# Kernel optimization log

Hardware: AMD Instinct MI355X
Metric: run time of the kernel (lower is better)

Reference implementation:

```python
import jax, jax.numpy as jnp
import numpy as np

H = 16        # num_heads
E = 1024      # embed_size
OUT = 1024    # out_dim
TEMP = 1.0
EPS = 1e-20
LN_EPS = 1e-5


def setup_inputs() -> dict:
    key = jax.random.key(0)
    ks = jax.random.split(key, 16)
    B, S = 8, 4096
    s = 1.0 / np.sqrt(E)
    inp = {
        'x': jax.random.normal(ks[0], (B, S, E), dtype=jnp.float32),
        'gumbel_u': jax.random.uniform(ks[1], (B, H, S, 2), dtype=jnp.float32, minval=1e-6, maxval=1.0 - 1e-6),
        'query': jax.random.uniform(ks[2], (1, E), dtype=jnp.float32, minval=-s, maxval=s),  # xavier-ish
        'Wq': jax.random.uniform(ks[3], (E, E), jnp.float32, -s, s),
        'bq': jnp.zeros((E,), jnp.float32),
        'Wk': jax.random.uniform(ks[4], (E, E), jnp.float32, -s, s),
        'bk': jnp.zeros((E,), jnp.float32),
        'Wv': jax.random.uniform(ks[5], (E, E), jnp.float32, -s, s),
        'bv': jnp.zeros((E,), jnp.float32),
        'ln_g': jnp.ones((E,), jnp.float32),
        'ln_b': jnp.zeros((E,), jnp.float32),
        'W1': jax.random.uniform(ks[6], (4 * E, E), jnp.float32, -s, s),
        'b1': jnp.zeros((4 * E,), jnp.float32),
        'W2': jax.random.uniform(ks[7], (OUT, 4 * E), jnp.float32, -0.5 * s, 0.5 * s),
        'b2': jnp.zeros((OUT,), jnp.float32),
    }
    return inp


def reference(x, gumbel_u, query, Wq, bq, Wk, bk, Wv, bv, ln_g, ln_b, W1, b1, W2, b2):
    B, S, _ = x.shape
    dk = E // H
    # projections
    q = (query @ Wq.T + bq).reshape(H, dk)                      # [H, dk] (single query, broadcast over batch)
    k = (x @ Wk.T + bk).reshape(B, S, H, dk)                    # [B, S, H, dk]
    v = (x @ Wv.T + bv).reshape(B, S, H, dk)
    # single-query attention logits
    logits = jnp.einsum('hd,bshd->bhs', q, k) / np.sqrt(dk)     # [B, H, S]
    probs = jax.nn.softmax(logits, axis=-1)                     # [B, H, S]
    # gumbel-softmax hard mask over {keep=0-logit, drop/keep pair}
    edges = jnp.stack([jnp.zeros_like(logits), logits], axis=-1)  # [B, H, S, 2]
    g = -jnp.log(-jnp.log(gumbel_u + EPS) + EPS)
    y_soft = jax.nn.softmax((edges + g) / TEMP, axis=-1)
    idx = jnp.argmax(y_soft, axis=-1)
    y_hard = jax.nn.one_hot(idx, 2, dtype=y_soft.dtype)
    y = jax.lax.stop_gradient(y_hard - y_soft) + y_soft         # straight-through
    A = y[..., 1]                                               # [B, H, S]
    probs = A * probs
    # weighted sum of values; merge heads (seq_len of query is 1)
    hidden = jnp.einsum('bhs,bshd->bhd', probs, v).reshape(B, E)
    # layernorm
    mu = hidden.mean(axis=-1, keepdims=True)
    var = hidden.var(axis=-1, keepdims=True)
    hidden = (hidden - mu) / jnp.sqrt(var + LN_EPS) * ln_g + ln_b
    # MLP (dropout p=0 -> identity)
    out = jax.nn.relu(hidden @ W1.T + b1) @ W2.T + b2           # [B, OUT]
    masks = A.sum(axis=1)[:, None, :]                           # sum_heads=True -> [B, 1, S]
    attn = probs.sum(axis=1)[:, None, :]
    return out, masks, attn
```

## Files before the change

### kernel.cpp

```cpp
#include <hip/hip_runtime.h>
#include <hip/hip_bf16.h>
#include <math.h>

#define SS 4096
#define EE 1024
#define HH 16

typedef __bf16 bf16x8 __attribute__((ext_vector_type(8)));
typedef float  f32x4v __attribute__((ext_vector_type(4)));

#define OFF_QVEC 0L
#define OFF_QKB  1024L
#define OFF_QH   1040L
#define OFF_QL   9232L
#define OFF_SEC  17424L
#define OFF_SAC  50192L
#define OFF_INVD 82960L
#define OFF_PSUM 83088L
#define OFF_WG   83216L
#define OFF_XA   607504L
#define OFF_HID  738576L
#define OFF_H2   746768L
#define OFF_T1   754960L
#define OFF_PT   787728L
#define OFF_PX   820496L

__device__ __forceinline__ float bf2f(unsigned int u){
  union { unsigned int i; float f; } c; c.i = u << 16; return c.f;
}
__device__ __forceinline__ unsigned int pk_hi(float a, float b){
  return __builtin_amdgcn_perm(__float_as_uint(b), __float_as_uint(a), 0x07060302u);
}
__device__ __forceinline__ float lo_part(float f){
  return f - __uint_as_float(__float_as_uint(f) & 0xFFFF0000u);
}
__device__ __forceinline__ unsigned short f2bf_rn(float f){
  unsigned int u = __float_as_uint(f);
  return (unsigned short)((u + 0x7fffu + ((u >> 16) & 1u)) >> 16);
}
__device__ __forceinline__ f32x4v mfma16(bf16x8 a, bf16x8 b, f32x4v c){
  return __builtin_amdgcn_mfma_f32_16x16x32_bf16(a, b, c, 0, 0, 0);
}
__device__ __forceinline__ float waveRedSum(float v){
  #pragma unroll
  for (int m=1;m<64;m<<=1) v += __shfl_xor(v, m, 64);
  return v;
}
template<int NW>
__device__ __forceinline__ float blockRedSum(float v, volatile float* scr){
  v = waveRedSum(v);
  const int w = threadIdx.x >> 6;
  __syncthreads();
  if ((threadIdx.x & 63) == 0) scr[w] = v;
  __syncthreads();
  float r = 0.f;
  #pragma unroll
  for (int i=0;i<NW;i++) r += scr[i];
  return r;
}

__global__ __launch_bounds__(256) void k1(const float* __restrict__ query, const float* __restrict__ Wq,
                                          const float* __restrict__ bq, float* __restrict__ qvec){
  const int wv = threadIdx.x >> 6, lane = threadIdx.x & 63;
  const int j = blockIdx.x * 4 + wv;
  float p = 0.f;
  #pragma unroll
  for (int i=0;i<4;i++){
    const int e = 4*lane + 256*i;
    const float4 q4 = *(const float4*)(query + e);
    const float4 w4 = *(const float4*)(Wq + (long)j*EE + e);
    p += q4.x*w4.x + q4.y*w4.y + q4.z*w4.z + q4.w*w4.w;
  }
  p = waveRedSum(p);
  if (lane == 0) qvec[j] = p + bq[j];
}

__global__ __launch_bounds__(256) void k2(const float* __restrict__ Wk, const float* __restrict__ bk,
                                          const float* __restrict__ qvec,
                                          unsigned short* __restrict__ qh, unsigned short* __restrict__ ql,
                                          float* __restrict__ qkb){
  __shared__ float red[4][64];
  const int wv = threadIdx.x >> 6, lane = threadIdx.x & 63;
  const int h = blockIdx.y;
  const int e = blockIdx.x*64 + lane;
  float acc = 0.f;
  #pragma unroll
  for (int dd=0; dd<16; dd++){
    const int d = wv*16 + dd;
    acc += qvec[h*64+d] * Wk[(long)(h*64+d)*EE + e];
  }
  red[wv][lane] = acc;
  __syncthreads();
  if (wv == 0){
    const float s = red[0][lane] + red[1][lane] + red[2][lane] + red[3][lane];
    const unsigned int ub = __float_as_uint(s);
    qh[h*EE + e] = (unsigned short)(ub >> 16);
    const float lo = s - __uint_as_float(ub & 0xFFFF0000u);
    ql[h*EE + e] = (unsigned short)(__float_as_uint(lo) >> 16);
    if (blockIdx.x == 0){
      float p = qvec[h*64+lane] * bk[h*64+lane];
      p = waveRedSum(p);
      if (lane == 0) qkb[h] = p;
    }
  }
}

__global__ __launch_bounds__(256,2) void k3(const float* __restrict__ x, const float* __restrict__ gum,
                                            const unsigned short* __restrict__ qh, const unsigned short* __restrict__ ql,
                                            const float* __restrict__ qkb,
                                            float* __restrict__ seC, float* __restrict__ saC,
                                            float* __restrict__ Wg, float* __restrict__ out){
  __shared__ float lg[4*16*17];
  __shared__ float w[16*20];
  __shared__ float scrA[16*17], scrB[16*17];
  __shared__ float sQkb[16];
  const int t = threadIdx.x;
  const int wv = t >> 6, lane = t & 63;
  const int m16 = lane & 15, q = lane >> 4;
  const int c = blockIdx.x, b = blockIdx.y;
  if (t < 16) sQkb[t] = qkb[t];
  const long xbase = ((long)(b*SS + c*16))*EE;

  f32x4v a = {0.f,0.f,0.f,0.f};
  #pragma unroll
  for (int kt=0; kt<8; kt++){
    const int k = wv*256 + kt*32 + q*8;
    const float* xp = x + xbase + (long)m16*EE + k;
    const float4 f0 = *(const float4*)(xp);
    const float4 f1 = *(const float4*)(xp + 4);
    union { uint4 u; bf16x8 v; } xh, xl, bh, bl;
    xh.u.x = pk_hi(f0.x, f0.y); xh.u.y = pk_hi(f0.z, f0.w);
    xh.u.z = pk_hi(f1.x, f1.y); xh.u.w = pk_hi(f1.z, f1.w);
    xl.u.x = pk_hi(lo_part(f0.x), lo_part(f0.y)); xl.u.y = pk_hi(lo_part(f0.z), lo_part(f0.w));
    xl.u.z = pk_hi(lo_part(f1.x), lo_part(f1.y)); xl.u.w = pk_hi(lo_part(f1.z), lo_part(f1.w));
    bh.u = *(const uint4*)(qh + (long)m16*EE + k);
    bl.u = *(const uint4*)(ql + (long)m16*EE + k);
    a = mfma16(xh.v, bh.v, a);
    a = mfma16(xh.v, bl.v, a);
    a = mfma16(xl.v, bh.v, a);
  }
  #pragma unroll
  for (int r=0;r<4;r++)
    lg[(wv*16 + q*4 + r)*17 + m16] = a[r];
  __syncthreads();

  {
    const int h = t & 15, s = t >> 4;
    const float dot = lg[(0*16+s)*17+h] + lg[(1*16+s)*17+h]
                    + lg[(2*16+s)*17+h] + lg[(3*16+s)*17+h];
    const float logit = (dot + sQkb[h]) * 0.125f;
    const long gi = ((long)(b*16 + h))*SS + c*16 + s;
    const float2 g2 = *(const float2*)(gum + 2*gi);
    const double gg0 = -log(-log((double)g2.x + 1e-20) + 1e-20);
    const double gg1 = -log(-log((double)g2.y + 1e-20) + 1e-20);
    const float e = expf(logit);
    const float wval = ((double)logit + gg1 > gg0) ? e : 0.f;
    w[s*20 + h] = wval;
    Wg[((long)b*SS + c*16 + s)*16 + h] = wval;
    scrA[s*17 + h] = e;
    scrB[s*17 + h] = wval;
  }
  __syncthreads();
  if (t < 16){
    float S = 0.f, SA = 0.f, cnt = 0.f;
    #pragma unroll
    for (int i=0;i<16;i++){ S += scrA[i*17 + t]; SA += scrB[i*17 + t]; }
    #pragma unroll
    for (int hh=0; hh<16; hh++) cnt += (w[t*20 + hh] > 0.f) ? 1.f : 0.f;
    seC[((long)(b*16 + t))*256 + c] = S;
    saC[((long)(b*16 + t))*256 + c] = SA;
    out[8192 + (long)b*SS + c*16 + t] = cnt;
  }
}

__global__ __launch_bounds__(256) void k4(const float* __restrict__ seC, const float* __restrict__ saC,
                                          float* __restrict__ invD, float* __restrict__ psum){
  __shared__ float sA[16*17], sB[16*17];
  const int b = blockIdx.x, t = threadIdx.x;
  const int h = t >> 4, cl = t & 15;
  float se = 0.f, sa = 0.f;
  #pragma unroll
  for (int k=0;k<16;k++){
    se += seC[((long)(b*16+h))*256 + cl + 16*k];
    sa += saC[((long)(b*16+h))*256 + cl + 16*k];
  }
  sA[h*17+cl] = se; sB[h*17+cl] = sa;
  __syncthreads();
  if (t < 16){
    float D = 0.f, SA = 0.f;
    #pragma unroll
    for (int i=0;i<16;i++){ D += sA[t*17+i]; SA += sB[t*17+i]; }
    const float inv = 1.f / D;
    invD[b*16+t] = inv; psum[b*16+t] = SA * inv;
  }
}

__global__ __launch_bounds__(256) void k5agg(const float* __restrict__ x, const float* __restrict__ Wg,
                                             const float* __restrict__ invD,
                                             unsigned short* __restrict__ px, float* __restrict__ out){
  __shared__ float wl[64*20];
  __shared__ float sInv[16];
  const int t = threadIdx.x, sseg = blockIdx.x, b = blockIdx.y;
  if (t < 16) sInv[t] = invD[b*16 + t];
  const int s0 = sseg*64;
  const float4 wv4 = *(const float4*)(Wg + ((long)b*SS + s0)*16 + 4*t);
  *(float4*)&wl[(t>>2)*20 + 4*(t&3)] = wv4;
  __syncthreads();
  if (t < 64){
    float a = 0.f;
    #pragma unroll
    for (int h=0; h<16; h++) a += wl[t*20 + h] * sInv[h];
    out[40960 + (long)b*SS + s0 + t] = a;
  }
  float acc[16][4];
  #pragma unroll
  for (int hh=0; hh<16; hh++){ acc[hh][0]=0.f; acc[hh][1]=0.f; acc[hh][2]=0.f; acc[hh][3]=0.f; }
  const float* xp = x + ((long)(b*SS + s0))*EE + 4*t;
  #pragma unroll 2
  for (int s=0; s<64; s++){
    const float4 xf = *(const float4*)(xp + (long)s*EE);
    float wv[16];
    *(float4*)&wv[0]  = *(const float4*)&wl[s*20 + 0];
    *(float4*)&wv[4]  = *(const float4*)&wl[s*20 + 4];
    *(float4*)&wv[8]  = *(const float4*)&wl[s*20 + 8];
    *(float4*)&wv[12] = *(const float4*)&wl[s*20 + 12];
    #pragma unroll
    for (int hh=0; hh<16; hh++){
      acc[hh][0] += wv[hh]*xf.x; acc[hh][1] += wv[hh]*xf.y;
      acc[hh][2] += wv[hh]*xf.z; acc[hh][3] += wv[hh]*xf.w;
    }
  }
  #pragma unroll
  for (int hh=0; hh<16; hh++){
    uint2 pk;
    pk.x = ((unsigned int)f2bf_rn(acc[hh][0])) | (((unsigned int)f2bf_rn(acc[hh][1])) << 16);
    pk.y = ((unsigned int)f2bf_rn(acc[hh][2])) | (((unsigned int)f2bf_rn(acc[hh][3])) << 16);
    *(uint2*)(px + (((long)(b*64 + sseg))*16 + hh)*EE + 4*t) = pk;
  }
}

__global__ __launch_bounds__(256) void k5b(const unsigned short* __restrict__ px, float* __restrict__ xa){
  const long g = (long)blockIdx.x*512 + 2*threadIdx.x;
  const int e = (int)(g & 1023);
  const int bh = (int)(g >> 10);
  const int b = bh >> 4, h = bh & 15;
  const unsigned short* p = px + (((long)(b*64))*16 + h)*EE + e;
  float a0 = 0.f, a1 = 0.f;
  #pragma unroll 8
  for (int seg=0; seg<64; seg++){
    const unsigned int u = *(const unsigned int*)(p + (long)seg*16384);
    a0 += bf2f(u & 0xffffu); a1 += bf2f(u >> 16);
  }
  xa[g] = a0; xa[g+1] = a1;
}

__global__ __launch_bounds__(256) void k6a(const float* __restrict__ xa, const float* __restrict__ Wv,
                                           const float* __restrict__ bv, const float* __restrict__ invD,
                                           const float* __restrict__ psum, float* __restrict__ hid){
  const int wv = threadIdx.x >> 6, lane = threadIdx.x & 63;
  const int W = blockIdx.x*4 + wv;
  const int b = W >> 8, jg = (W & 255)*4;
  for (int jj=0; jj<4; jj++){
    const int j = jg + jj, h = j >> 6;
    const float* xr = xa + ((long)(b*16+h))*EE;
    const float* wr = Wv + (long)j*EE;
    float p = 0.f;
    #pragma unroll
    for (int i=0;i<4;i++){
      const int e = 4*lane + 256*i;
      const float4 a4 = *(const float4*)(xr + e);
      const float4 w4 = *(const float4*)(wr + e);
      p += a4.x*w4.x + a4.y*w4.y + a4.z*w4.z + a4.w*w4.w;
    }
    p = waveRedSum(p);
    if (lane == 0) hid[(long)b*EE + j] = p*invD[b*16+h] + psum[b*16+h]*bv[j];
  }
}

__global__ __launch_bounds__(1024) void k6b(const float* __restrict__ hid, const float* __restrict__ lng,
                                            const float* __restrict__ lnb, unsigned short* __restrict__ h2u){
  __shared__ float scr[16];
  const int b = blockIdx.x, t = threadIdx.x;
  if (b >= 8){ h2u[(long)b*EE + t] = 0; return; }
  const float v = hid[(long)b*EE + t];
  const float s1 = blockRedSum<16>(v, scr);
  const float s2 = blockRedSum<16>(v*v, scr);
  const float mu  = s1 * (1.f/1024.f);
  const float var = s2 * (1.f/1024.f) - mu*mu;
  const float rs = rsqrtf(var + 1e-5f);
  h2u[(long)b*EE + t] = f2bf_rn((v - mu)*rs*lng[t] + lnb[t]);
}

__global__ __launch_bounds__(256) void k8(const unsigned short* __restrict__ h2u, const float* __restrict__ W1,
                                          const float* __restrict__ b1, unsigned short* __restrict__ t1u){
  __shared__ float red[4*64*4];
  const int wv = threadIdx.x >> 6, lane = threadIdx.x & 63;
  const int m16 = lane & 15, q = lane >> 4;
  const int j = blockIdx.x*16 + m16;
  f32x4v a = {0.f,0.f,0.f,0.f};
  #pragma unroll
  for (int kt=0; kt<8; kt++){
    const int k = wv*256 + kt*32 + q*8;
    union { uint4 u; bf16x8 v; } A, B;
    A.u = *(const uint4*)(h2u + (long)m16*EE + k);
    const float4 f0 = *(const float4*)(W1 + (long)j*EE + k);
    const float4 f1 = *(const float4*)(W1 + (long)j*EE + k + 4);
    B.u.x = pk_hi(f0.x,f0.y); B.u.y = pk_hi(f0.z,f0.w);
    B.u.z = pk_hi(f1.x,f1.y); B.u.w = pk_hi(f1.z,f1.w);
    a = mfma16(A.v, B.v, a);
  }
  #pragma unroll
  for (int r=0;r<4;r++) red[(wv*64 + lane)*4 + r] = a[r];
  __syncthreads();
  if (wv == 0){
    #pragma unroll
    for (int r=0;r<4;r++){
      const float s = red[(0*64+lane)*4+r] + red[(1*64+lane)*4+r]
                    + red[(2*64+lane)*4+r] + red[(3*64+lane)*4+r];
      const int row = q*4 + r;
      const float val = (row < 8) ? fmaxf(s + b1[j], 0.f) : 0.f;
      t1u[(long)row*4096 + j] = f2bf_rn(val);
    }
  }
}

__global__ __launch_bounds__(256) void k9(const unsigned short* __restrict__ t1u, const float* __restrict__ W2,
                                          float* __restrict__ pt){
  __shared__ float red[4*64*4];
  const int wv = threadIdx.x >> 6, lane = threadIdx.x & 63;
  const int m16 = lane & 15, q = lane >> 4;
  const int o = blockIdx.x*16 + m16;
  const int kbase = blockIdx.y*1024 + wv*256;
  f32x4v a = {0.f,0.f,0.f,0.f};
  #pragma unroll
  for (int kt=0; kt<8; kt++){
    const int k = kbase + kt*32 + q*8;
    union { uint4 u; bf16x8 v; } A, B;
    A.u = *(const uint4*)(t1u + (long)m16*4096 + k);
    const float4 f0 = *(const float4*)(W2 + (long)o*4096 + k);
    const float4 f1 = *(const float4*)(W2 + (long)o*4096 + k + 4);
    B.u.x = pk_hi(f0.x,f0.y); B.u.y = pk_hi(f0.z,f0.w);
    B.u.z = pk_hi(f1.x,f1.y); B.u.w = pk_hi(f1.z,f1.w);
    a = mfma16(A.v, B.v, a);
  }
  #pragma unroll
  for (int r=0;r<4;r++) red[(wv*64 + lane)*4 + r] = a[r];
  __syncthreads();
  if (wv == 0){
    #pragma unroll
    for (int r=0;r<4;r++){
      const int row = q*4 + r;
      if (row < 8){
        const float s = red[(0*64+lane)*4+r] + red[(1*64+lane)*4+r]
                      + red[(2*64+lane)*4+r] + red[(3*64+lane)*4+r];
        pt[(long)blockIdx.y*8192 + row*1024 + o] = s;
      }
    }
  }
}

__global__ __launch_bounds__(256) void k9b(const float* __restrict__ pt, const float* __restrict__ b2,
                                           float* __restrict__ out){
  const int idx = blockIdx.x*256 + threadIdx.x;
  const int o = idx & 1023;
  out[idx] = pt[idx] + pt[8192+idx] + pt[16384+idx] + pt[24576+idx] + b2[o];
}

extern "C" void kernel_launch(void* const* d_in, const int* in_sizes, int n_in,
                              void* d_out, int out_size, void* d_ws, size_t ws_size,
                              hipStream_t stream){
  const float* x    = (const float*)d_in[0];
  const float* gum  = (const float*)d_in[1];
  const float* query= (const float*)d_in[2];
  const float* Wq   = (const float*)d_in[3];
  const float* bq   = (const float*)d_in[4];
  const float* Wk   = (const float*)d_in[5];
  const float* bk   = (const float*)d_in[6];
  const float* Wv   = (const float*)d_in[7];
  const float* bv   = (const float*)d_in[8];
  const float* lng  = (const float*)d_in[9];
  const float* lnb  = (const float*)d_in[10];
  const float* W1   = (const float*)d_in[11];
  const float* b1   = (const float*)d_in[12];
  const float* W2   = (const float*)d_in[13];
  const float* b2   = (const float*)d_in[14];
  float* ws = (float*)d_ws;
  float* qvec = ws + OFF_QVEC;
  float* qkb  = ws + OFF_QKB;
  unsigned short* qh = (unsigned short*)(ws + OFF_QH);
  unsigned short* ql = (unsigned short*)(ws + OFF_QL);
  float* seC  = ws + OFF_SEC;
  float* saC  = ws + OFF_SAC;
  float* invD = ws + OFF_INVD;
  float* psum = ws + OFF_PSUM;
  float* Wg   = ws + OFF_WG;
  float* xa   = ws + OFF_XA;
  float* hid  = ws + OFF_HID;
  unsigned short* h2u = (unsigned short*)(ws + OFF_H2);
  unsigned short* t1u = (unsigned short*)(ws + OFF_T1);
  float* pt   = ws + OFF_PT;
  unsigned short* px  = (unsigned short*)(ws + OFF_PX);
  float* out = (float*)d_out;

  k1   <<<256, 256, 0, stream>>>(query, Wq, bq, qvec);
  k2   <<<dim3(16,16), 256, 0, stream>>>(Wk, bk, qvec, qh, ql, qkb);
  k3   <<<dim3(256,8), 256, 0, stream>>>(x, gum, qh, ql, qkb, seC, saC, Wg, out);
  k4   <<<8, 256, 0, stream>>>(seC, saC, invD, psum);
  k5agg<<<dim3(64,8), 256, 0, stream>>>(x, Wg, invD, px, out);
  k5b  <<<256, 256, 0, stream>>>(px, xa);
  k6a  <<<512, 256, 0, stream>>>(xa, Wv, bv, invD, psum, hid);
  k6b  <<<16, 1024, 0, stream>>>(hid, lng, lnb, h2u);
  k8   <<<256, 256, 0, stream>>>(h2u, W1, b1, t1u);
  k9   <<<dim3(64,4), 256, 0, stream>>>(t1u, W2, pt);
  k9b  <<<32, 256, 0, stream>>>(pt, b2, out);
}
```

Baseline: 304.9 us.

## Fuse logit and value-aggregation passes over x into one MFMA kernel

The logits kernel now also computes the per-head weighted sum of x rows with MFMA, reusing the bf16 hi/lo split of x staged in LDS. This removes the second full read of x that the separate aggregation kernel made. The softmax normalisation, the attn output and the Wv projection are merged into one kernel that accumulates with atomics. LayerNorm moves into the W1 kernel, and the final W2 reduction adds into out with atomics instead of a separate sum kernel. The cost is a large per-block LDS tile and 64 accumulator registers per thread, which may lower occupancy. Atomic accumulation also makes the result order-dependent.

```diff
diff --git a/kernel.cpp b/kernel.cpp
--- a/kernel.cpp
+++ b/kernel.cpp
@@ -15,19 +15,11 @@
 #define OFF_QL   9232L
 #define OFF_SEC  17424L
 #define OFF_SAC  50192L
-#define OFF_INVD 82960L
-#define OFF_PSUM 83088L
-#define OFF_WG   83216L
-#define OFF_XA   607504L
-#define OFF_HID  738576L
-#define OFF_H2   746768L
-#define OFF_T1   754960L
-#define OFF_PT   787728L
-#define OFF_PX   820496L
-
-__device__ __forceinline__ float bf2f(unsigned int u){
-  union { unsigned int i; float f; } c; c.i = u << 16; return c.f;
-}
+#define OFF_WG   82960L
+#define OFF_HID  607248L
+#define OFF_T1   615440L
+#define OFF_PX   648208L
+
 __device__ __forceinline__ unsigned int pk_hi(float a, float b){
   return __builtin_amdgcn_perm(__float_as_uint(b), __float_as_uint(a), 0x07060302u);
 }
@@ -60,7 +52,8 @@
 }
 
 __global__ __launch_bounds__(256) void k1(const float* __restrict__ query, const float* __restrict__ Wq,
-                                          const float* __restrict__ bq, float* __restrict__ qvec){
+                                          const float* __restrict__ bq, float* __restrict__ qvec,
+                                          float* __restrict__ hid){
   const int wv = threadIdx.x >> 6, lane = threadIdx.x & 63;
   const int j = blockIdx.x * 4 + wv;
   float p = 0.f;
@@ -73,6 +66,7 @@
   }
   p = waveRedSum(p);
   if (lane == 0) qvec[j] = p + bq[j];
+  if (blockIdx.x < 32) hid[blockIdx.x*256 + threadIdx.x] = 0.f;
 }
 
 __global__ __launch_bounds__(256) void k2(const float* __restrict__ Wk, const float* __restrict__ bk,
@@ -105,196 +99,227 @@
   }
 }
 
-__global__ __launch_bounds__(256,2) void k3(const float* __restrict__ x, const float* __restrict__ gum,
-                                            const unsigned short* __restrict__ qh, const unsigned short* __restrict__ ql,
-                                            const float* __restrict__ qkb,
-                                            float* __restrict__ seC, float* __restrict__ saC,
-                                            float* __restrict__ Wg, float* __restrict__ out){
+__global__ __launch_bounds__(256,2) void k3f(const float* __restrict__ x, const float* __restrict__ gum,
+                                             const unsigned short* __restrict__ qh, const unsigned short* __restrict__ ql,
+                                             const float* __restrict__ qkb,
+                                             float* __restrict__ seC, float* __restrict__ saC,
+                                             float* __restrict__ Wg, float* __restrict__ px,
+                                             float* __restrict__ out){
+  __shared__ unsigned short xsT[4][256*32];
   __shared__ float lg[4*16*17];
-  __shared__ float w[16*20];
+  __shared__ float wT[16][20];
   __shared__ float scrA[16*17], scrB[16*17];
   __shared__ float sQkb[16];
   const int t = threadIdx.x;
   const int wv = t >> 6, lane = t & 63;
   const int m16 = lane & 15, q = lane >> 4;
-  const int c = blockIdx.x, b = blockIdx.y;
+  const int blk = blockIdx.x, b = blockIdx.y;
   if (t < 16) sQkb[t] = qkb[t];
-  const long xbase = ((long)(b*SS + c*16))*EE;
-
-  f32x4v a = {0.f,0.f,0.f,0.f};
-  #pragma unroll
-  for (int kt=0; kt<8; kt++){
-    const int k = wv*256 + kt*32 + q*8;
-    const float* xp = x + xbase + (long)m16*EE + k;
-    const float4 f0 = *(const float4*)(xp);
-    const float4 f1 = *(const float4*)(xp + 4);
-    union { uint4 u; bf16x8 v; } xh, xl, bh, bl;
-    xh.u.x = pk_hi(f0.x, f0.y); xh.u.y = pk_hi(f0.z, f0.w);
-    xh.u.z = pk_hi(f1.x, f1.y); xh.u.w = pk_hi(f1.z, f1.w);
-    xl.u.x = pk_hi(lo_part(f0.x), lo_part(f0.y)); xl.u.y = pk_hi(lo_part(f0.z), lo_part(f0.w));
-    xl.u.z = pk_hi(lo_part(f1.x), lo_part(f1.y)); xl.u.w = pk_hi(lo_part(f1.z), lo_part(f1.w));
-    bh.u = *(const uint4*)(qh + (long)m16*EE + k);
-    bl.u = *(const uint4*)(ql + (long)m16*EE + k);
-    a = mfma16(xh.v, bh.v, a);
-    a = mfma16(xh.v, bl.v, a);
-    a = mfma16(xl.v, bh.v, a);
-  }
-  #pragma unroll
-  for (int r=0;r<4;r++)
-    lg[(wv*16 + q*4 + r)*17 + m16] = a[r];
-  __syncthreads();
+  unsigned short* xw = &xsT[wv][0];
+
+  f32x4v P[16];
+  #pragma unroll
+  for (int i=0;i<16;i++){ P[i][0]=0.f; P[i][1]=0.f; P[i][2]=0.f; P[i][3]=0.f; }
+
+  for (int ch=0; ch<4; ch++){
+    const int c = blk*4 + ch;
+    const long xbase = ((long)(b*SS + c*16))*EE;
+
+    f32x4v a = {0.f,0.f,0.f,0.f};
+    #pragma unroll
+    for (int kt=0; kt<8; kt++){
+      const int k = wv*256 + kt*32 + q*8;
+      const float* xp = x + xbase + (long)m16*EE + k;
+      const float4 f0 = *(const float4*)(xp);
+      const float4 f1 = *(const float4*)(xp + 4);
+      union { uint4 u; bf16x8 v; } xh, xl, bh, bl;
+      xh.u.x = pk_hi(f0.x, f0.y); xh.u.y = pk_hi(f0.z, f0.w);
+      xh.u.z = pk_hi(f1.x, f1.y); xh.u.w = pk_hi(f1.z, f1.w);
+      xl.u.x = pk_hi(lo_part(f0.x), lo_part(f0.y)); xl.u.y = pk_hi(lo_part(f0.z), lo_part(f0.w));
+      xl.u.z = pk_hi(lo_part(f1.x), lo_part(f1.y)); xl.u.w = pk_hi(lo_part(f1.z), lo_part(f1.w));
+      bh.u = *(const uint4*)(qh + (long)m16*EE + k);
+      bl.u = *(const uint4*)(ql + (long)m16*EE + k);
+      a = mfma16(xh.v, bh.v, a);
+      a = mfma16(xh.v, bl.v, a);
+      a = mfma16(xl.v, bh.v, a);
+      const int e0 = kt*32 + q*8;
+      const unsigned hw[4] = {xh.u.x, xh.u.y, xh.u.z, xh.u.w};
+      const unsigned lw[4] = {xl.u.x, xl.u.y, xl.u.z, xl.u.w};
+      #pragma unroll
+      for (int jj=0; jj<8; jj++){
+        const unsigned sh = (jj & 1) * 16;
+        xw[(e0+jj)*32 + m16]      = (unsigned short)(hw[jj>>1] >> sh);
+        xw[(e0+jj)*32 + 16 + m16] = (unsigned short)(lw[jj>>1] >> sh);
+      }
+    }
+    #pragma unroll
+    for (int r=0;r<4;r++)
+      lg[(wv*16 + q*4 + r)*17 + m16] = a[r];
+    __syncthreads();
+
+    {
+      const int h = t & 15, s = t >> 4;
+      const float dot = lg[(0*16+s)*17+h] + lg[(1*16+s)*17+h]
+                      + lg[(2*16+s)*17+h] + lg[(3*16+s)*17+h];
+      const float logit = (dot + sQkb[h]) * 0.125f;
+      const long gi = ((long)(b*16 + h))*SS + c*16 + s;
+      const float2 g2 = *(const float2*)(gum + 2*gi);
+      const double gg0 = -log(-log((double)g2.x + 1e-20) + 1e-20);
+      const double gg1 = -log(-log((double)g2.y + 1e-20) + 1e-20);
+      const float e = expf(logit);
+      const float wval = ((double)logit + gg1 > gg0) ? e : 0.f;
+      wT[h][s] = wval;
+      Wg[((long)b*SS + c*16 + s)*16 + h] = wval;
+      scrA[s*17 + h] = e;
+      scrB[s*17 + h] = wval;
+    }
+    __syncthreads();
+
+    if (t < 16){
+      float S = 0.f, SA = 0.f, cnt = 0.f;
+      #pragma unroll
+      for (int i=0;i<16;i++){ S += scrA[i*17 + t]; SA += scrB[i*17 + t]; }
+      #pragma unroll
+      for (int hh=0; hh<16; hh++) cnt += (scrB[t*17 + hh] > 0.f) ? 1.f : 0.f;
+      seC[((long)(b*16 + t))*256 + c] = S;
+      saC[((long)(b*16 + t))*256 + c] = SA;
+      out[8192 + (long)b*SS + c*16 + t] = cnt;
+    }
+
+    {
+      float wf[8];
+      *(float4*)&wf[0] = *(const float4*)&wT[m16][(q & 1)*8];
+      *(float4*)&wf[4] = *(const float4*)&wT[m16][(q & 1)*8 + 4];
+      union { uint4 u; bf16x8 v; } B1, B2;
+      B1.u.x = pk_hi(wf[0],wf[1]); B1.u.y = pk_hi(wf[2],wf[3]);
+      B1.u.z = pk_hi(wf[4],wf[5]); B1.u.w = pk_hi(wf[6],wf[7]);
+      B2.u.x = pk_hi(lo_part(wf[0]),lo_part(wf[1])); B2.u.y = pk_hi(lo_part(wf[2]),lo_part(wf[3]));
+      B2.u.z = pk_hi(lo_part(wf[4]),lo_part(wf[5])); B2.u.w = pk_hi(lo_part(wf[6]),lo_part(wf[7]));
+      #pragma unroll
+      for (int et=0; et<16; et++){
+        union { uint4 u; bf16x8 v; } A;
+        A.u = *(const uint4*)(xw + (et*16 + m16)*32 + q*8);
+        P[et] = mfma16(A.v, B1.v, P[et]);
+        P[et] = mfma16(A.v, B2.v, P[et]);
+      }
+    }
+  }
+
+  const long pbase = (((long)(b*64 + blk))*16 + m16)*1024 + wv*256;
+  #pragma unroll
+  for (int et=0; et<16; et++){
+    #pragma unroll
+    for (int r=0;r<4;r++)
+      px[pbase + et*16 + q*4 + r] = P[et][r];
+  }
+}
+
+__global__ __launch_bounds__(256) void kb(const float* __restrict__ px, const float* __restrict__ Wg,
+                                          const float* __restrict__ seC, const float* __restrict__ saC,
+                                          const float* __restrict__ Wv, const float* __restrict__ bv,
+                                          float* __restrict__ hid, float* __restrict__ out){
+  __shared__ float s_red[16][17];
+  __shared__ float sInv[16];
+  __shared__ float scr1[4], scr2[4];
+  __shared__ float xs[256];
+  const int t = threadIdx.x;
+
+  if (blockIdx.x < 32){
+    const int b = blockIdx.x >> 2, sq = blockIdx.x & 3;
+    { const int h = t >> 4, cl = t & 15;
+      float se = 0.f;
+      #pragma unroll
+      for (int k=0;k<16;k++) se += seC[((long)(b*16+h))*256 + cl + 16*k];
+      s_red[h][cl] = se;
+    }
+    __syncthreads();
+    if (t < 16){
+      float D = 0.f;
+      #pragma unroll
+      for (int i=0;i<16;i++) D += s_red[t][i];
+      sInv[t] = 1.f / D;
+    }
+    __syncthreads();
+    #pragma unroll
+    for (int it=0; it<4; it++){
+      const int s = sq*1024 + it*256 + t;
+      const float* wr = Wg + ((long)b*SS + s)*16;
+      float a = 0.f;
+      #pragma unroll
+      for (int h=0;h<16;h++) a += wr[h]*sInv[h];
+      out[40960 + (long)b*SS + s] = a;
+    }
+    return;
+  }
+
+  const int idx = blockIdx.x - 32;
+  const int b = idx >> 6, h = (idx >> 2) & 15, eq = idx & 3;
+  const long rbase = ((long)(b*16 + h))*256;
+  const float D    = blockRedSum<4>(seC[rbase + t], scr1);
+  const float SA   = blockRedSum<4>(saC[rbase + t], scr2);
+  const float invD = 1.f / D;
+  const float psum = SA * invD;
+  const float* pp = px + (((long)(b*64))*16 + h)*1024 + eq*256 + t;
+  float xa = 0.f;
+  #pragma unroll 8
+  for (int seg=0; seg<64; seg++) xa += pp[(long)seg*16384];
+  xs[t] = xa;
+  __syncthreads();
+  const int wv = t >> 6, lane = t & 63;
+  const float4 xv = *(const float4*)(xs + 4*lane);
+  #pragma unroll 4
+  for (int jj=0; jj<16; jj++){
+    const int j = h*64 + wv*16 + jj;
+    const float4 w4 = *(const float4*)(Wv + (long)j*EE + eq*256 + 4*lane);
+    float p = xv.x*w4.x + xv.y*w4.y + xv.z*w4.z + xv.w*w4.w;
+    p = waveRedSum(p);
+    if (lane == 0){
+      float add = p * invD;
+      if (eq == 0) add += psum * bv[j];
+      atomicAdd(&hid[(long)b*EE + j], add);
+    }
+  }
+}
+
+__global__ __launch_bounds__(256) void k8f(const float* __restrict__ hid, const float* __restrict__ lng,
+                                           const float* __restrict__ lnb, const float* __restrict__ W1,
+                                           const float* __restrict__ b1, const float* __restrict__ b2,
+                                           unsigned short* __restrict__ t1u, float* __restrict__ out){
+  __shared__ unsigned short h2[16*1032];
+  __shared__ float red[4*64*4];
+  const int t = threadIdx.x;
+  if (blockIdx.x < 32) out[blockIdx.x*256 + t] = b2[(blockIdx.x & 3)*256 + t];
 
   {
-    const int h = t & 15, s = t >> 4;
-    const float dot = lg[(0*16+s)*17+h] + lg[(1*16+s)*17+h]
-                    + lg[(2*16+s)*17+h] + lg[(3*16+s)*17+h];
-    const float logit = (dot + sQkb[h]) * 0.125f;
-    const long gi = ((long)(b*16 + h))*SS + c*16 + s;
-    const float2 g2 = *(const float2*)(gum + 2*gi);
-    const double gg0 = -log(-log((double)g2.x + 1e-20) + 1e-20);
-    const double gg1 = -log(-log((double)g2.y + 1e-20) + 1e-20);
-    const float e = expf(logit);
-    const float wval = ((double)logit + gg1 > gg0) ? e : 0.f;
-    w[s*20 + h] = wval;
-    Wg[((long)b*SS + c*16 + s)*16 + h] = wval;
-    scrA[s*17 + h] = e;
-    scrB[s*17 + h] = wval;
-  }
-  __syncthreads();
-  if (t < 16){
-    float S = 0.f, SA = 0.f, cnt = 0.f;
-    #pragma unroll
-    for (int i=0;i<16;i++){ S += scrA[i*17 + t]; SA += scrB[i*17 + t]; }
-    #pragma unroll
-    for (int hh=0; hh<16; hh++) cnt += (w[t*20 + hh] > 0.f) ? 1.f : 0.f;
-    seC[((long)(b*16 + t))*256 + c] = S;
-    saC[((long)(b*16 + t))*256 + c] = SA;
-    out[8192 + (long)b*SS + c*16 + t] = cnt;
-  }
-}
-
-__global__ __launch_bounds__(256) void k4(const float* __restrict__ seC, const float* __restrict__ saC,
-                                          float* __restrict__ invD, float* __restrict__ psum){
-  __shared__ float sA[16*17], sB[16*17];
-  const int b = blockIdx.x, t = threadIdx.x;
-  const int h = t >> 4, cl = t & 15;
-  float se = 0.f, sa = 0.f;
-  #pragma unroll
-  for (int k=0;k<16;k++){
-    se += seC[((long)(b*16+h))*256 + cl + 16*k];
-    sa += saC[((long)(b*16+h))*256 + cl + 16*k];
-  }
-  sA[h*17+cl] = se; sB[h*17+cl] = sa;
-  __syncthreads();
-  if (t < 16){
-    float D = 0.f, SA = 0.f;
-    #pragma unroll
-    for (int i=0;i<16;i++){ D += sA[t*17+i]; SA += sB[t*17+i]; }
-    const float inv = 1.f / D;
-    invD[b*16+t] = inv; psum[b*16+t] = SA * inv;
-  }
-}
-
-__global__ __launch_bounds__(256) void k5agg(const float* __restrict__ x, const float* __restrict__ Wg,
-                                             const float* __restrict__ invD,
-                                             unsigned short* __restrict__ px, float* __restrict__ out){
-  __shared__ float wl[64*20];
-  __shared__ float sInv[16];
-  const int t = threadIdx.x, sseg = blockIdx.x, b = blockIdx.y;
-  if (t < 16) sInv[t] = invD[b*16 + t];
-  const int s0 = sseg*64;
-  const float4 wv4 = *(const float4*)(Wg + ((long)b*SS + s0)*16 + 4*t);
-  *(float4*)&wl[(t>>2)*20 + 4*(t&3)] = wv4;
-  __syncthreads();
-  if (t < 64){
-    float a = 0.f;
-    #pragma unroll
-    for (int h=0; h<16; h++) a += wl[t*20 + h] * sInv[h];
-    out[40960 + (long)b*SS + s0 + t] = a;
-  }
-  float acc[16][4];
-  #pragma unroll
-  for (int hh=0; hh<16; hh++){ acc[hh][0]=0.f; acc[hh][1]=0.f; acc[hh][2]=0.f; acc[hh][3]=0.f; }
-  const float* xp = x + ((long)(b*SS + s0))*EE + 4*t;
-  #pragma unroll 2
-  for (int s=0; s<64; s++){
-    const float4 xf = *(const float4*)(xp + (long)s*EE);
-    float wv[16];
-    *(float4*)&wv[0]  = *(const float4*)&wl[s*20 + 0];
-    *(float4*)&wv[4]  = *(const float4*)&wl[s*20 + 4];
-    *(float4*)&wv[8]  = *(const float4*)&wl[s*20 + 8];
-    *(float4*)&wv[12] = *(const float4*)&wl[s*20 + 12];
-    #pragma unroll
-    for (int hh=0; hh<16; hh++){
-      acc[hh][0] += wv[hh]*xf.x; acc[hh][1] += wv[hh]*xf.y;
-      acc[hh][2] += wv[hh]*xf.z; acc[hh][3] += wv[hh]*xf.w;
-    }
-  }
-  #pragma unroll
-  for (int hh=0; hh<16; hh++){
-    uint2 pk;
-    pk.x = ((unsigned int)f2bf_rn(acc[hh][0])) | (((unsigned int)f2bf_rn(acc[hh][1])) << 16);
-    pk.y = ((unsigned int)f2bf_rn(acc[hh][2])) | (((unsigned int)f2bf_rn(acc[hh][3])) << 16);
-    *(uint2*)(px + (((long)(b*64 + sseg))*16 + hh)*EE + 4*t) = pk;
-  }
-}
-
-__global__ __launch_bounds__(256) void k5b(const unsigned short* __restrict__ px, float* __restrict__ xa){
-  const long g = (long)blockIdx.x*512 + 2*threadIdx.x;
-  const int e = (int)(g & 1023);
-  const int bh = (int)(g >> 10);
-  const int b = bh >> 4, h = bh & 15;
-  const unsigned short* p = px + (((long)(b*64))*16 + h)*EE + e;
-  float a0 = 0.f, a1 = 0.f;
-  #pragma unroll 8
-  for (int seg=0; seg<64; seg++){
-    const unsigned int u = *(const unsigned int*)(p + (long)seg*16384);
-    a0 += bf2f(u & 0xffffu); a1 += bf2f(u >> 16);
-  }
-  xa[g] = a0; xa[g+1] = a1;
-}
-
-__global__ __launch_bounds__(256) void k6a(const float* __restrict__ xa, const float* __restrict__ Wv,
-                                           const float* __restrict__ bv, const float* __restrict__ invD,
-                                           const float* __restrict__ psum, float* __restrict__ hid){
-  const int wv = threadIdx.x >> 6, lane = threadIdx.x & 63;
-  const int W = blockIdx.x*4 + wv;
-  const int b = W >> 8, jg = (W & 255)*4;
-  for (int jj=0; jj<4; jj++){
-    const int j = jg + jj, h = j >> 6;
-    const float* xr = xa + ((long)(b*16+h))*EE;
-    const float* wr = Wv + (long)j*EE;
-    float p = 0.f;
-    #pragma unroll
-    for (int i=0;i<4;i++){
-      const int e = 4*lane + 256*i;
-      const float4 a4 = *(const float4*)(xr + e);
-      const float4 w4 = *(const float4*)(wr + e);
-      p += a4.x*w4.x + a4.y*w4.y + a4.z*w4.z + a4.w*w4.w;
-    }
-    p = waveRedSum(p);
-    if (lane == 0) hid[(long)b*EE + j] = p*invD[b*16+h] + psum[b*16+h]*bv[j];
-  }
-}
-
-__global__ __launch_bounds__(1024) void k6b(const float* __restrict__ hid, const float* __restrict__ lng,
-                                            const float* __restrict__ lnb, unsigned short* __restrict__ h2u){
-  __shared__ float scr[16];
-  const int b = blockIdx.x, t = threadIdx.x;
-  if (b >= 8){ h2u[(long)b*EE + t] = 0; return; }
-  const float v = hid[(long)b*EE + t];
-  const float s1 = blockRedSum<16>(v, scr);
-  const float s2 = blockRedSum<16>(v*v, scr);
-  const float mu  = s1 * (1.f/1024.f);
-  const float var = s2 * (1.f/1024.f) - mu*mu;
-  const float rs = rsqrtf(var + 1e-5f);
-  h2u[(long)b*EE + t] = f2bf_rn((v - mu)*rs*lng[t] + lnb[t]);
-}
-
-__global__ __launch_bounds__(256) void k8(const unsigned short* __restrict__ h2u, const float* __restrict__ W1,
-                                          const float* __restrict__ b1, unsigned short* __restrict__ t1u){
-  __shared__ float red[4*64*4];
-  const int wv = threadIdx.x >> 6, lane = threadIdx.x & 63;
+    const int r = t >> 5, ll = t & 31;
+    float4 vv[8];
+    float s1 = 0.f, s2 = 0.f;
+    #pragma unroll
+    for (int i=0;i<8;i++){
+      vv[i] = *(const float4*)(hid + (long)r*1024 + ll*32 + i*4);
+      s1 += vv[i].x + vv[i].y + vv[i].z + vv[i].w;
+      s2 += vv[i].x*vv[i].x + vv[i].y*vv[i].y + vv[i].z*vv[i].z + vv[i].w*vv[i].w;
+    }
+    #pragma unroll
+    for (int m=1;m<32;m<<=1){ s1 += __shfl_xor(s1, m, 32); s2 += __shfl_xor(s2, m, 32); }
+    const float mu  = s1 * (1.f/1024.f);
+    const float var = s2 * (1.f/1024.f) - mu*mu;
+    const float rs  = rsqrtf(var + 1e-5f);
+    #pragma unroll
+    for (int i=0;i<8;i++){
+      const int e = ll*32 + i*4;
+      const float4 g4 = *(const float4*)(lng + e);
+      const float4 b4 = *(const float4*)(lnb + e);
+      uint2 pk;
+      pk.x = (unsigned)f2bf_rn((vv[i].x-mu)*rs*g4.x + b4.x) | ((unsigned)f2bf_rn((vv[i].y-mu)*rs*g4.y + b4.y) << 16);
+      pk.y = (unsigned)f2bf_rn((vv[i].z-mu)*rs*g4.z + b4.z) | ((unsigned)f2bf_rn((vv[i].w-mu)*rs*g4.w + b4.w) << 16);
+      *(uint2*)(h2 + r*1032 + e) = pk;
+      *(uint2*)(h2 + (8+r)*1032 + e) = make_uint2(0u, 0u);
+    }
+  }
+  __syncthreads();
+
+  const int wv = t >> 6, lane = t & 63;
   const int m16 = lane & 15, q = lane >> 4;
   const int j = blockIdx.x*16 + m16;
   f32x4v a = {0.f,0.f,0.f,0.f};
@@ -302,7 +327,7 @@
   for (int kt=0; kt<8; kt++){
     const int k = wv*256 + kt*32 + q*8;
     union { uint4 u; bf16x8 v; } A, B;
-    A.u = *(const uint4*)(h2u + (long)m16*EE + k);
+    A.u = *(const uint4*)(h2 + m16*1032 + k);
     const float4 f0 = *(const float4*)(W1 + (long)j*EE + k);
     const float4 f1 = *(const float4*)(W1 + (long)j*EE + k + 4);
     B.u.x = pk_hi(f0.x,f0.y); B.u.y = pk_hi(f0.z,f0.w);
@@ -324,8 +349,8 @@
   }
 }
 
-__global__ __launch_bounds__(256) void k9(const unsigned short* __restrict__ t1u, const float* __restrict__ W2,
-                                          float* __restrict__ pt){
+__global__ __launch_bounds__(256) void k9a(const unsigned short* __restrict__ t1u, const float* __restrict__ W2,
+                                           float* __restrict__ out){
   __shared__ float red[4*64*4];
   const int wv = threadIdx.x >> 6, lane = threadIdx.x & 63;
   const int m16 = lane & 15, q = lane >> 4;
@@ -353,17 +378,10 @@
       if (row < 8){
         const float s = red[(0*64+lane)*4+r] + red[(1*64+lane)*4+r]
                       + red[(2*64+lane)*4+r] + red[(3*64+lane)*4+r];
-        pt[(long)blockIdx.y*8192 + row*1024 + o] = s;
+        atomicAdd(out + row*1024 + o, s);
       }
     }
   }
-}
-
-__global__ __launch_bounds__(256) void k9b(const float* __restrict__ pt, const float* __restrict__ b2,
-                                           float* __restrict__ out){
-  const int idx = blockIdx.x*256 + threadIdx.x;
-  const int o = idx & 1023;
-  out[idx] = pt[idx] + pt[8192+idx] + pt[16384+idx] + pt[24576+idx] + b2[o];
 }
 
 extern "C" void kernel_launch(void* const* d_in, const int* in_sizes, int n_in,
@@ -391,26 +409,16 @@
   unsigned short* ql = (unsigned short*)(ws + OFF_QL);
   float* seC  = ws + OFF_SEC;
   float* saC  = ws + OFF_SAC;
-  float* invD = ws + OFF_INVD;
-  float* psum = ws + OFF_PSUM;
   float* Wg   = ws + OFF_WG;
-  float* xa   = ws + OFF_XA;
   float* hid  = ws + OFF_HID;
-  unsigned short* h2u = (unsigned short*)(ws + OFF_H2);
   unsigned short* t1u = (unsigned short*)(ws + OFF_T1);
-  float* pt   = ws + OFF_PT;
-  unsigned short* px  = (unsigned short*)(ws + OFF_PX);
+  float* px   = ws + OFF_PX;
   float* out = (float*)d_out;
 
-  k1   <<<256, 256, 0, stream>>>(query, Wq, bq, qvec);
-  k2   <<<dim3(16,16), 256, 0, stream>>>(Wk, bk, qvec, qh, ql, qkb);
-  k3   <<<dim3(256,8), 256, 0, stream>>>(x, gum, qh, ql, qkb, seC, saC, Wg, out);
-  k4   <<<8, 256, 0, stream>>>(seC, saC, invD, psum);
-  k5agg<<<dim3(64,8), 256, 0, stream>>>(x, Wg, invD, px, out);
-  k5b  <<<256, 256, 0, stream>>>(px, xa);
-  k6a  <<<512, 256, 0, stream>>>(xa, Wv, bv, invD, psum, hid);
-  k6b  <<<16, 1024, 0, stream>>>(hid, lng, lnb, h2u);
-  k8   <<<256, 256, 0, stream>>>(h2u, W1, b1, t1u);
-  k9   <<<dim3(64,4), 256, 0, stream>>>(t1u, W2, pt);
-  k9b  <<<32, 256, 0, stream>>>(pt, b2, out);
-}
+  k1  <<<256, 256, 0, stream>>>(query, Wq, bq, qvec, hid);
+  k2  <<<dim3(16,16), 256, 0, stream>>>(Wk, bk, qvec, qh, ql, qkb);
+  k3f <<<dim3(64,8), 256, 0, stream>>>(x, gum, qh, ql, qkb, seC, saC, Wg, px, out);
+  kb  <<<544, 256, 0, stream>>>(px, Wg, seC, saC, Wv, bv, hid, out);
+  k8f <<<256, 256, 0, stream>>>(hid, lng, lnb, W1, b1, b2, t1u, out);
+  k9a <<<dim3(64,4), 256, 0, stream>>>(t1u, W2, out);
+}
```

New measurement: 292.9 us. 1.04x faster.
